# Performance work log

Hardware: AMD Instinct MI355X
Metric: run time of the kernel (lower is better)

## Reference

```python
import jax, jax.numpy as jnp
import numpy as np

PSA_TYPE = 0  # 0 = 'collect', 1 = 'distribute'
H_MASK = 97
W_MASK = 97


def psamask(x, psa_type, h_mask, w_mask):
    """Faithful JAX port of mmcv PSAMask.
    collect:    out[b, nh*W+nw, h, w] = x[b, (nh-h+hh)*wm + (nw-w+hw), h, w]
    distribute: out[b, h*W+w, nh, nw] = x[b, (nh-h+hh)*wm + (nw-w+hw), h, w]
    where hh=(h_mask-1)//2, hw=(w_mask-1)//2 and entries outside the local
    mask window are zero.
    """
    B, C, H, W = x.shape
    half_h = (h_mask - 1) // 2
    half_w = (w_mask - 1) // 2
    h = jnp.arange(H)
    w = jnp.arange(W)
    # hidx[nh, h] = mask row index for neighbor nh of pixel row h
    hidx = h[:, None] - h[None, :] + half_h          # (H, H)
    widx = w[:, None] - w[None, :] + half_w          # (W, W)
    vh = (hidx >= 0) & (hidx < h_mask)
    vw = (widx >= 0) & (widx < w_mask)
    hc = jnp.clip(hidx, 0, h_mask - 1).astype(jnp.int32)
    wc = jnp.clip(widx, 0, w_mask - 1).astype(jnp.int32)
    if psa_type == 0:
        # output layout (nh, nw, h, w)
        cidx = hc[:, None, :, None] * w_mask + wc[None, :, None, :]   # (H, W, H, W)
        valid = vh[:, None, :, None] & vw[None, :, None, :]
        out = x[:, cidx, h[None, None, :, None], w[None, None, None, :]]  # (B, H, W, H, W)
    else:
        # output layout (h, w, nh, nw)
        cidx = hc.T[:, None, :, None] * w_mask + wc.T[None, :, None, :]
        valid = vh.T[:, None, :, None] & vw.T[None, :, None, :]
        out = x[:, cidx, h[:, None, None, None], w[None, :, None, None]]
    out = jnp.where(valid[None], out, 0.0)
    return out.reshape(B, H * W, H, W)


def setup_inputs() -> dict:
    key = jax.random.key(0)
    B, H, W = 1, 97, 97
    x = jax.random.normal(key, (B, H_MASK * W_MASK, H, W), dtype=jnp.float32)
    return {"x": x}


def reference(x):
    return psamask(x, PSA_TYPE, H_MASK, W_MASK)
```

## Files before the change

### kernel.cpp

```cpp
#include <hip/hip_runtime.h>


#define HW    97
#define PLANE 9409
#define HALF  48
#define NT    512
#define NITER 19

typedef const __attribute__((address_space(1))) void* gptr_t;
typedef __attribute__((address_space(3))) void* lptr_t;

__global__ __launch_bounds__(NT)
void psamask_collect_kernel(const float* __restrict__ x, float* __restrict__ out) {
    const int h  = blockIdx.x;
    const int nh = blockIdx.y;
    const int a  = nh - h + HALF;
    const unsigned tid = threadIdx.x;

    float* __restrict__ outp = out + (size_t)(nh * HW) * PLANE + h * HW;

    const unsigned r0 = tid / HW;
    const unsigned c0 = tid - r0 * HW;

    if ((unsigned)a >= HW) {
        unsigned w   = c0;
        unsigned off = r0 * PLANE + c0;
        #pragma unroll
        for (int k = 0; k < NITER; ++k) {
            unsigned d = tid + (unsigned)k * NT;
            if (d < PLANE) outp[off] = 0.0f;
            w += 27;
            bool wrap = (w >= HW);
            off += wrap ? (6u * PLANE - 70u) : (5u * PLANE + 27u);
            if (wrap) w -= HW;
        }
        return;
    }

    __shared__ float lds[PLANE];

    const float* __restrict__ xp = x + (size_t)(a * HW) * PLANE + h * HW;
    {
        unsigned b = r0, cw = c0;
        #pragma unroll
        for (int k = 0; k < NITER; ++k) {
            unsigned d = tid + (unsigned)k * NT;
            if (d < PLANE) {
                unsigned w = cw - b + ((cw < b) ? HW : 0u);
                const float* g = xp + b * PLANE + w;
                unsigned d0 = (unsigned)k * NT + (tid & ~63u);
                __builtin_amdgcn_global_load_lds((gptr_t)g, (lptr_t)&lds[d0], 4, 0, 0);
            }
            b += 5; cw += 27;
            if (cw >= HW) { cw -= HW; b += 1; }
        }
    }
    asm volatile("s_waitcnt vmcnt(0)" ::: "memory");
    __syncthreads();

    {
        unsigned w   = c0;
        int      b   = (int)r0 - (int)c0 + HALF;
        unsigned cw  = r0 + HALF; if (cw >= HW) cw -= HW;
        unsigned off = r0 * PLANE + c0;
        #pragma unroll
        for (int k = 0; k < NITER; ++k) {
            unsigned d = tid + (unsigned)k * NT;
            if (d < PLANE) {
                bool valid = ((unsigned)b < HW);
                unsigned bc = valid ? (unsigned)b : 0u;
                float v = lds[bc * HW + cw];
                outp[off] = valid ? v : 0.0f;
            }
            w += 27;
            bool wrap = (w >= HW);
            if (wrap) w -= HW;
            b  += wrap ? 76 : -22;
            cw += wrap ? 6u : 5u;
            if (cw >= HW) cw -= HW;
            off += wrap ? (6u * PLANE - 70u) : (5u * PLANE + 27u);
        }
    }
}

extern "C" void kernel_launch(void* const* d_in, const int* in_sizes, int n_in,
                              void* d_out, int out_size, void* d_ws, size_t ws_size,
                              hipStream_t stream) {
    const float* x = (const float*)d_in[0];
    float* out = (float*)d_out;
    dim3 grid(HW, HW);
    psamask_collect_kernel<<<grid, NT, 0, stream>>>(x, out);
}
```

Baseline: 184.2 us.

## Process multiple h rows per block with a persistent loop over chunks

The grid shrinks from 97x97 blocks to 97x16, and each block loops over 6-7 consecutive h rows, reusing one LDS buffer with barriers between iterations. The aim is to cut block launch and scheduling overhead and amortise setup. Rows whose window falls outside the mask now run through the same path with zero-writes instead of an early exit. This serialises load and store phases within a block and leaves only 1552 blocks, which could lower memory-level parallelism on a bandwidth-bound write kernel.

```diff
diff --git a/kernel.cpp b/kernel.cpp
--- a/kernel.cpp
+++ b/kernel.cpp
@@ -12,73 +12,68 @@
 
 __global__ __launch_bounds__(NT)
 void psamask_collect_kernel(const float* __restrict__ x, float* __restrict__ out) {
-    const int h  = blockIdx.x;
-    const int nh = blockIdx.y;
-    const int a  = nh - h + HALF;
+    const int nh = blockIdx.x;
+    const int c  = blockIdx.y;
+    const int h0 = (c == 0) ? 0 : 7 + (c - 1) * 6;
+    const int TH = (c == 0) ? 7 : 6;
     const unsigned tid = threadIdx.x;
-
-    float* __restrict__ outp = out + (size_t)(nh * HW) * PLANE + h * HW;
 
     const unsigned r0 = tid / HW;
     const unsigned c0 = tid - r0 * HW;
 
-    if ((unsigned)a >= HW) {
-        unsigned w   = c0;
-        unsigned off = r0 * PLANE + c0;
-        #pragma unroll
-        for (int k = 0; k < NITER; ++k) {
-            unsigned d = tid + (unsigned)k * NT;
-            if (d < PLANE) outp[off] = 0.0f;
-            w += 27;
-            bool wrap = (w >= HW);
-            off += wrap ? (6u * PLANE - 70u) : (5u * PLANE + 27u);
-            if (wrap) w -= HW;
-        }
-        return;
-    }
-
     __shared__ float lds[PLANE];
 
-    const float* __restrict__ xp = x + (size_t)(a * HW) * PLANE + h * HW;
-    {
-        unsigned b = r0, cw = c0;
-        #pragma unroll
-        for (int k = 0; k < NITER; ++k) {
-            unsigned d = tid + (unsigned)k * NT;
-            if (d < PLANE) {
-                unsigned w = cw - b + ((cw < b) ? HW : 0u);
-                const float* g = xp + b * PLANE + w;
-                unsigned d0 = (unsigned)k * NT + (tid & ~63u);
-                __builtin_amdgcn_global_load_lds((gptr_t)g, (lptr_t)&lds[d0], 4, 0, 0);
+    for (int t = 0; t < TH; ++t) {
+        const int h = h0 + t;
+        const int a = nh - h + HALF;
+        const bool avalid = ((unsigned)a < HW);
+
+        if (t) __syncthreads();
+
+        if (avalid) {
+            const float* __restrict__ xp =
+                x + (size_t)((unsigned)a * HW) * PLANE + (unsigned)h * HW;
+            unsigned b = r0, cw = c0;
+            #pragma unroll
+            for (int k = 0; k < NITER; ++k) {
+                unsigned d = tid + (unsigned)k * NT;
+                if (d < PLANE) {
+                    unsigned w = cw - b + ((cw < b) ? HW : 0u);
+                    const float* g = xp + b * PLANE + w;
+                    unsigned d0 = (unsigned)k * NT + (tid & ~63u);
+                    __builtin_amdgcn_global_load_lds((gptr_t)g, (lptr_t)&lds[d0], 4, 0, 0);
+                }
+                b += 5; cw += 27;
+                if (cw >= HW) { cw -= HW; b += 1; }
             }
-            b += 5; cw += 27;
-            if (cw >= HW) { cw -= HW; b += 1; }
         }
-    }
-    asm volatile("s_waitcnt vmcnt(0)" ::: "memory");
-    __syncthreads();
+        asm volatile("s_waitcnt vmcnt(0)" ::: "memory");
+        __syncthreads();
 
-    {
-        unsigned w   = c0;
-        int      b   = (int)r0 - (int)c0 + HALF;
-        unsigned cw  = r0 + HALF; if (cw >= HW) cw -= HW;
-        unsigned off = r0 * PLANE + c0;
-        #pragma unroll
-        for (int k = 0; k < NITER; ++k) {
-            unsigned d = tid + (unsigned)k * NT;
-            if (d < PLANE) {
-                bool valid = ((unsigned)b < HW);
-                unsigned bc = valid ? (unsigned)b : 0u;
-                float v = lds[bc * HW + cw];
-                outp[off] = valid ? v : 0.0f;
+        {
+            float* __restrict__ outp =
+                out + (size_t)((unsigned)nh * HW) * PLANE + (unsigned)h * HW;
+            unsigned w   = c0;
+            int      b   = (int)r0 - (int)c0 + HALF;
+            unsigned cw  = r0 + HALF; if (cw >= HW) cw -= HW;
+            unsigned off = r0 * PLANE + c0;
+            #pragma unroll
+            for (int k = 0; k < NITER; ++k) {
+                unsigned d = tid + (unsigned)k * NT;
+                if (d < PLANE) {
+                    bool valid = avalid && ((unsigned)b < HW);
+                    unsigned bc = ((unsigned)b < HW) ? (unsigned)b : 0u;
+                    float v = lds[bc * HW + cw];
+                    outp[off] = valid ? v : 0.0f;
+                }
+                w += 27;
+                bool wrap = (w >= HW);
+                if (wrap) w -= HW;
+                b  += wrap ? 76 : -22;
+                cw += wrap ? 6u : 5u;
+                if (cw >= HW) cw -= HW;
+                off += wrap ? (6u * PLANE - 70u) : (5u * PLANE + 27u);
             }
-            w += 27;
-            bool wrap = (w >= HW);
-            if (wrap) w -= HW;
-            b  += wrap ? 76 : -22;
-            cw += wrap ? 6u : 5u;
-            if (cw >= HW) cw -= HW;
-            off += wrap ? (6u * PLANE - 70u) : (5u * PLANE + 27u);
         }
     }
 }
@@ -88,6 +83,6 @@
                               hipStream_t stream) {
     const float* x = (const float*)d_in[0];
     float* out = (float*)d_out;
-    dim3 grid(HW, HW);
+    dim3 grid(HW, 16);
     psamask_collect_kernel<<<grid, NT, 0, stream>>>(x, out);
 }
```

Result: faster. 179.9 us (-2.4%).

## Use persistent XCD-aware blocks with double-buffered LDS staging of row pairs

Applied to the files above, without the earlier changes.

Replaces the 97x97 grid of one-row blocks with 512 persistent blocks. Each block walks a contiguous range of (nh, h-pair) slots, and slots are assigned per XCD by nh modulo 8. The next slot's inputs are prefetched into a second LDS buffer with global_load_lds while the current slot's values are held in registers and written out, so loads overlap stores. Invalid windows are still read from clamped addresses and masked to zero rather than skipped. The cost is higher register use, tricky hand-set vmcnt counts, and edge handling for the odd final row.

```diff
diff --git a/kernel.cpp b/kernel.cpp
--- a/kernel.cpp
+++ b/kernel.cpp
@@ -5,81 +5,116 @@
 #define PLANE 9409
 #define HALF  48
 #define NT    512
-#define NITER 19
+#define LNK   19
+#define PSTR  9728
+#define SNK   37
+#define SOFF_LAST (96*PLANE + 193)
+#define SRD_LAST  (PSTR + 48*HW + 47)
 
 typedef const __attribute__((address_space(1))) void* gptr_t;
 typedef __attribute__((address_space(3))) void* lptr_t;
 
-__global__ __launch_bounds__(NT)
-void psamask_collect_kernel(const float* __restrict__ x, float* __restrict__ out) {
-    const int h  = blockIdx.x;
-    const int nh = blockIdx.y;
-    const int a  = nh - h + HALF;
+__global__ __launch_bounds__(NT, 4)
+void psamask_pers2(const float* __restrict__ x, float* __restrict__ out) {
     const unsigned tid = threadIdx.x;
+    const unsigned xcd = blockIdx.x & 7u;
+    const unsigned j   = blockIdx.x >> 3;
+    const unsigned cnt = (xcd == 0u) ? 13u : 12u;
+    const unsigned T   = cnt * 49u;
+    const unsigned s0  = (j * T) >> 6;
+    const unsigned s1  = ((j + 1u) * T) >> 6;
+    const int nslot = (int)(s1 - s0);
 
-    float* __restrict__ outp = out + (size_t)(nh * HW) * PLANE + h * HW;
+    __shared__ float lds[2 * PSTR];
 
     const unsigned r0 = tid / HW;
     const unsigned c0 = tid - r0 * HW;
 
-    if ((unsigned)a >= HW) {
-        unsigned w   = c0;
-        unsigned off = r0 * PLANE + c0;
+    auto stage = [&](unsigned gs, unsigned cs) {
+        int nh = (int)(8u * gs + xcd);
+        int h0 = 2 * (int)cs; if (h0 > 95) h0 = 95;
+        int a0 = nh - h0 + HALF;
         #pragma unroll
-        for (int k = 0; k < NITER; ++k) {
-            unsigned d = tid + (unsigned)k * NT;
-            if (d < PLANE) outp[off] = 0.0f;
-            w += 27;
-            bool wrap = (w >= HW);
-            off += wrap ? (6u * PLANE - 70u) : (5u * PLANE + 27u);
-            if (wrap) w -= HW;
+        for (int p = 0; p < 2; ++p) {
+            int a = a0 - p;
+            unsigned ac = (a < 0) ? 0u : ((a > 96) ? 96u : (unsigned)a);
+            const float* xp = x + (size_t)(ac * HW) * PLANE + (unsigned)(h0 + p) * HW;
+            unsigned b = r0, cw = c0;
+            #pragma unroll
+            for (int k = 0; k < LNK; ++k) {
+                unsigned w = cw - b + ((cw < b) ? HW : 0u);
+                unsigned soffk = (k == LNK - 1 && tid >= 193u)
+                                   ? 0u : (b * PLANE + w);
+                unsigned d0 = (unsigned)p * PSTR + (unsigned)k * NT + (tid & ~63u);
+                __builtin_amdgcn_global_load_lds((gptr_t)(xp + soffk),
+                                                 (lptr_t)&lds[d0], 4, 0, 0);
+                b += 5; cw += 27;
+                if (cw >= HW) { cw -= HW; b += 1; }
+            }
         }
-        return;
-    }
+    };
 
-    __shared__ float lds[PLANE];
+    unsigned g = s0 / 49u, cc = s0 - g * 49u;
+    stage(g, cc);
+    asm volatile("s_waitcnt vmcnt(0)" ::: "memory");
+    __builtin_amdgcn_s_barrier();
 
-    const float* __restrict__ xp = x + (size_t)(a * HW) * PLANE + h * HW;
-    {
-        unsigned b = r0, cw = c0;
-        #pragma unroll
-        for (int k = 0; k < NITER; ++k) {
-            unsigned d = tid + (unsigned)k * NT;
-            if (d < PLANE) {
-                unsigned w = cw - b + ((cw < b) ? HW : 0u);
-                const float* g = xp + b * PLANE + w;
-                unsigned d0 = (unsigned)k * NT + (tid & ~63u);
-                __builtin_amdgcn_global_load_lds((gptr_t)g, (lptr_t)&lds[d0], 4, 0, 0);
+    for (int i = 0; i < nslot; ++i) {
+        const int nh = (int)(8u * g + xcd);
+        int h0 = 2 * (int)cc; if (h0 > 95) h0 = 95;
+        const int a0 = nh - h0 + HALF;
+        const unsigned av0 = ((unsigned)a0       < HW) ? 1u : 0u;
+        const unsigned av1 = ((unsigned)(a0 - 1) < HW) ? 1u : 0u;
+
+        float v[SNK];
+        {
+            unsigned q  = (tid >= 194u ? 1u : 0u) + (tid >= 388u ? 1u : 0u);
+            unsigned e  = tid - q * 194u;
+            unsigned cw = q + HALF;
+            #pragma unroll
+            for (int k = 0; k < SNK; ++k) {
+                unsigned hp = (e >= 97u) ? 1u : 0u;
+                unsigned w  = e - hp * 97u;
+                int b = (int)q - (int)w + HALF;
+                bool vb = ((unsigned)b < HW);
+                unsigned bc = vb ? (unsigned)b : 0u;
+                unsigned srd = hp * PSTR + bc * HW + cw;
+                unsigned av  = hp ? av1 : av0;
+                if (k == SNK - 1) {
+                    if (tid >= 386u) { srd = SRD_LAST; av = av1; vb = true; }
+                }
+                float val = lds[srd];
+                v[k] = (vb && av) ? val : 0.0f;
+                e += 124u; q += 2u; cw += 2u;
+                if (e >= 194u) { e -= 194u; q += 1u; cw += 1u; }
+                if (cw >= 97u) cw -= 97u;
             }
-            b += 5; cw += 27;
-            if (cw >= HW) { cw -= HW; b += 1; }
         }
-    }
-    asm volatile("s_waitcnt vmcnt(0)" ::: "memory");
-    __syncthreads();
+        asm volatile("s_waitcnt lgkmcnt(0)" ::: "memory");
+        __builtin_amdgcn_sched_barrier(0);
+        __builtin_amdgcn_s_barrier();
 
-    {
-        unsigned w   = c0;
-        int      b   = (int)r0 - (int)c0 + HALF;
-        unsigned cw  = r0 + HALF; if (cw >= HW) cw -= HW;
-        unsigned off = r0 * PLANE + c0;
-        #pragma unroll
-        for (int k = 0; k < NITER; ++k) {
-            unsigned d = tid + (unsigned)k * NT;
-            if (d < PLANE) {
-                bool valid = ((unsigned)b < HW);
-                unsigned bc = valid ? (unsigned)b : 0u;
-                float v = lds[bc * HW + cw];
-                outp[off] = valid ? v : 0.0f;
+        unsigned gn = g, cn = cc + 1u;
+        if (cn == 49u) { cn = 0u; gn += 1u; }
+        if (i + 1 < nslot) stage(gn, cn);
+
+        {
+            float* op = out + (size_t)((unsigned)nh * HW) * PLANE + (unsigned)h0 * HW;
+            unsigned q   = (tid >= 194u ? 1u : 0u) + (tid >= 388u ? 1u : 0u);
+            unsigned e   = tid - q * 194u;
+            unsigned off = q * PLANE + e;
+            #pragma unroll
+            for (int k = 0; k < SNK; ++k) {
+                unsigned offk = off;
+                if (k == SNK - 1 && tid >= 386u) offk = SOFF_LAST;
+                op[offk] = v[k];
+                e += 124u; q += 2u; off += 2u * PLANE + 124u;
+                if (e >= 194u) { e -= 194u; q += 1u; off += PLANE - 194u; }
             }
-            w += 27;
-            bool wrap = (w >= HW);
-            if (wrap) w -= HW;
-            b  += wrap ? 76 : -22;
-            cw += wrap ? 6u : 5u;
-            if (cw >= HW) cw -= HW;
-            off += wrap ? (6u * PLANE - 70u) : (5u * PLANE + 27u);
         }
+        asm volatile("s_waitcnt vmcnt(37)" ::: "memory");
+        __builtin_amdgcn_s_barrier();
+        g = gn; cc = cn;
     }
 }
 
@@ -88,6 +123,5 @@
                               hipStream_t stream) {
     const float* x = (const float*)d_in[0];
     float* out = (float*)d_out;
-    dim3 grid(HW, HW);
-    psamask_collect_kernel<<<grid, NT, 0, stream>>>(x, out);
+    psamask_pers2<<<dim3(512), NT, 0, stream>>>(x, out);
 }
```

Result: slower. 428.3 us (+132.5%).
